# Kernel tuning notes

Hardware: AMD Instinct MI355X
Metric: run time of the kernel (lower is better)

The kernel has to match this reference:

```python
import jax, jax.numpy as jnp
import numpy as np

NUM_HEADS = 8
CH_PER_HEAD = 32
NUM_GROUPS = 32
EPS = 1e-5
SCALE = CH_PER_HEAD ** (-0.25)


def group_norm(x, scale, bias):
    # x: [b, c, h, w]
    b, c, h, w = x.shape
    xg = x.reshape(b, NUM_GROUPS, c // NUM_GROUPS, h, w)
    mean = xg.mean(axis=(2, 3, 4), keepdims=True)
    var = xg.var(axis=(2, 3, 4), keepdims=True)
    xg = (xg - mean) * jax.lax.rsqrt(var + EPS)
    x = xg.reshape(b, c, h, w)
    return x * scale[None, :, None, None] + bias[None, :, None, None]


def conv1x1(x, w, b):
    # x: [b, c_in, n], w: [c_out, c_in], b: [c_out]
    return jnp.einsum('oc,bcn->bon', w, x) + b[None, :, None]


def setup_inputs() -> dict:
    key = jax.random.key(0)
    ks = jax.random.split(key, 12)
    c_in, c_out, hid = 256, 256, NUM_HEADS * CH_PER_HEAD
    d = {}
    d['x'] = jax.random.normal(ks[0], (2, c_in, 64, 64), dtype=jnp.float32)
    d['gn_scale'] = jnp.ones((c_in,), dtype=jnp.float32)
    d['gn_bias'] = jnp.zeros((c_in,), dtype=jnp.float32)
    def lin(k, co, ci):
        return jax.random.normal(k, (co, ci), dtype=jnp.float32) * (ci ** -0.5)
    d['wq'] = lin(ks[1], hid, c_in)
    d['bq'] = jnp.zeros((hid,), dtype=jnp.float32)
    d['wk'] = lin(ks[2], hid, c_in)
    d['bk'] = jnp.zeros((hid,), dtype=jnp.float32)
    d['wv'] = lin(ks[3], hid, c_in)
    d['bv'] = jnp.zeros((hid,), dtype=jnp.float32)
    # Original zero-inits to_out; we use small random weights so the
    # attention path contributes to the output (non-trivial baseline).
    d['wo'] = lin(ks[4], c_out, hid) * 0.02
    d['bo'] = jnp.zeros((c_out,), dtype=jnp.float32)
    return d


def reference(x, gn_scale, gn_bias, wq, bq, wk, bk, wv, bv, wo, bo):
    b, c, h, w = x.shape
    n = h * w
    x_n = group_norm(x, gn_scale, gn_bias).reshape(b, c, n)
    q = conv1x1(x_n, wq, bq)  # [b, hid, n]
    k = conv1x1(x_n, wk, bk)
    v = conv1x1(x_n, wv, bv)
    def split_heads(t):
        return t.reshape(b, NUM_HEADS, CH_PER_HEAD, n)
    q, k, v = split_heads(q) * SCALE, split_heads(k) * SCALE, split_heads(v)
    attn = jax.nn.softmax(jnp.einsum('bhdi,bhdj->bhij', q, k), axis=-1)
    out = jnp.einsum('bhij,bhdj->bhdi', attn, v)  # [b, h, d, n]
    out = out.reshape(b, NUM_HEADS * CH_PER_HEAD, n)
    out = conv1x1(out, wo, bo).reshape(b, -1, h, w)
    return x + out
```

## Files before the change

### kernel.cpp

```cpp
#include <hip/hip_runtime.h>

#define C 256
#define N 4096
#define CPG 8
#define GE (CPG * N)
#define JL 2048

constexpr float EPS = 1e-5f;
constexpr float QK_SCALE_E = 0.50500979f;

typedef float f32x4 __attribute__((ext_vector_type(4)));
typedef short s16x8 __attribute__((ext_vector_type(8)));

__device__ __forceinline__ short f2bf(float f) {
    union { float f; unsigned u; } v; v.f = f;
    unsigned r = v.u + 0x7FFFu + ((v.u >> 16) & 1u);
    return (short)(r >> 16);
}
__device__ __forceinline__ float bf2f(short s) {
    union { unsigned u; float f; } v; v.u = ((unsigned)(unsigned short)s) << 16;
    return v.f;
}

__global__ __launch_bounds__(1024) void k_stats(const float* __restrict__ x,
                                                float2* __restrict__ stats) {
    int b = blockIdx.x >> 5, g = blockIdx.x & 31;
    size_t base = (size_t)(b * C + g * CPG) * N;
    const float* xp = x + base;
    int tid = threadIdx.x;
    float sum = 0.f, ss = 0.f;
    for (int i = tid * 4; i < GE; i += 4096) {
        float4 v = *(const float4*)(xp + i);
        sum += (v.x + v.y) + (v.z + v.w);
        ss  += (v.x * v.x + v.y * v.y) + (v.z * v.z + v.w * v.w);
    }
    #pragma unroll
    for (int o = 32; o; o >>= 1) {
        sum += __shfl_down(sum, o, 64);
        ss  += __shfl_down(ss, o, 64);
    }
    __shared__ float red[32];
    int wid = tid >> 6;
    if ((tid & 63) == 0) { red[wid] = sum; red[16 + wid] = ss; }
    __syncthreads();
    if (tid == 0) {
        sum = 0.f; ss = 0.f;
        #pragma unroll
        for (int i = 0; i < 16; ++i) { sum += red[i]; ss += red[16 + i]; }
        float mean = sum * (1.f / GE);
        float var  = ss * (1.f / GE) - mean * mean;
        stats[b * 32 + g] = make_float2(mean, rsqrtf(var + EPS));
    }
}

__global__ __launch_bounds__(256) void k_wcvt(const float* __restrict__ wq,
        const float* __restrict__ wk, const float* __restrict__ wv,
        const float* __restrict__ wo, short* __restrict__ wqkvb,
        short* __restrict__ wob) {
    int i = blockIdx.x * 256 + threadIdx.x;
    if (i < 65536)       wqkvb[i] = f2bf(wq[i]);
    else if (i < 131072) wqkvb[i] = f2bf(wk[i - 65536]);
    else if (i < 196608) wqkvb[i] = f2bf(wv[i - 131072]);
    else                 wob[i - 196608] = f2bf(wo[i - 196608]);
}

__global__ __launch_bounds__(256) void k_t(const float* __restrict__ x,
        const float* __restrict__ gs, const float* __restrict__ gb,
        const float2* __restrict__ stats, short* __restrict__ xnT) {
    __shared__ __align__(16) short lt[64][72];
    int id = blockIdx.x;
    int b  = id >> 8;
    int ct = (id >> 6) & 3;
    int nt = id & 63;
    int c0 = ct * 64, n0 = nt * 64;
    int t = threadIdx.x;
    int cc = t >> 2;
    int c = c0 + cc;
    float2 st = stats[b * 32 + (c >> 3)];
    float sc = gs[c] * st.y;
    float bi = gb[c] - st.x * sc;
    const float* xp = x + (size_t)(b * C + c) * N + n0;
    #pragma unroll
    for (int it = 0; it < 4; ++it) {
        int f4 = (t & 3) + it * 4;
        float4 v = *(const float4*)(xp + f4 * 4);
        int nl = f4 * 4;
        lt[nl + 0][cc] = f2bf(v.x * sc + bi);
        lt[nl + 1][cc] = f2bf(v.y * sc + bi);
        lt[nl + 2][cc] = f2bf(v.z * sc + bi);
        lt[nl + 3][cc] = f2bf(v.w * sc + bi);
    }
    __syncthreads();
    int nl = t >> 2, seg = t & 3;
    short* op = xnT + (size_t)(b * N + n0 + nl) * C + c0 + seg * 16;
    s16x8 w0 = *(const s16x8*)&lt[nl][seg * 16];
    s16x8 w1 = *(const s16x8*)&lt[nl][seg * 16 + 8];
    *(s16x8*)op = w0;
    *(s16x8*)(op + 8) = w1;
}

__global__ __launch_bounds__(256) void k_qkv(const short* __restrict__ wqkvb,
        const short* __restrict__ xnT, const float* __restrict__ bq,
        const float* __restrict__ bk, const float* __restrict__ bv,
        short* __restrict__ qT, short* __restrict__ kT, short* __restrict__ vB) {
    __shared__ __align__(16) short lt[4][64][16];
    int nb = blockIdx.x, mb = blockIdx.y, b = blockIdx.z;
    int m0 = mb * 64, n0 = nb * 64;
    int wid = threadIdx.x >> 6, lane = threadIdx.x & 63;
    int lr = lane & 15, lg = lane >> 4;
    int mw = m0 + wid * 16;
    const short* ap_ = wqkvb + (mw + lr) * C + lg * 8;
    const short* bp_ = xnT + ((size_t)b * N + n0 + lr) * C + lg * 8;
    f32x4 acc[4] = {{0,0,0,0},{0,0,0,0},{0,0,0,0},{0,0,0,0}};
    #pragma unroll 4
    for (int k0 = 0; k0 < C; k0 += 32) {
        s16x8 a  = *(const s16x8*)(ap_ + k0);
        s16x8 x0 = *(const s16x8*)(bp_ + k0);
        s16x8 x1 = *(const s16x8*)(bp_ + 16 * C + k0);
        s16x8 x2 = *(const s16x8*)(bp_ + 32 * C + k0);
        s16x8 x3 = *(const s16x8*)(bp_ + 48 * C + k0);
        acc[0] = __builtin_amdgcn_mfma_f32_16x16x32_bf16(a, x0, acc[0], 0, 0, 0);
        acc[1] = __builtin_amdgcn_mfma_f32_16x16x32_bf16(a, x1, acc[1], 0, 0, 0);
        acc[2] = __builtin_amdgcn_mfma_f32_16x16x32_bf16(a, x2, acc[2], 0, 0, 0);
        acc[3] = __builtin_amdgcn_mfma_f32_16x16x32_bf16(a, x3, acc[3], 0, 0, 0);
    }
    int kind = mb >> 2;
    const float* bias = kind == 0 ? bq : (kind == 1 ? bk : bv);
    int mloc = mw - kind * 256;
    float bvals[4];
    #pragma unroll
    for (int r = 0; r < 4; ++r) bvals[r] = bias[mloc + 4 * lg + r];
    int h = mloc >> 5;
    if (kind == 2) {
        short* vbase = vB + (size_t)((b * 8 + h) * 32) * N;
        #pragma unroll
        for (int f = 0; f < 4; ++f) {
            int n = n0 + f * 16 + lr;
            #pragma unroll
            for (int r = 0; r < 4; ++r) {
                int dd = (mloc & 31) + 4 * lg + r;
                vbase[(size_t)dd * N + n] = f2bf(acc[f][r] + bvals[r]);
            }
        }
    } else {
        short* dst = (kind == 0) ? qT : kT;
        #pragma unroll
        for (int f = 0; f < 4; ++f)
            #pragma unroll
            for (int r = 0; r < 4; ++r)
                lt[wid][f * 16 + lr][4 * lg + r] =
                    f2bf((acc[f][r] + bvals[r]) * QK_SCALE_E);
        int ln = lane;
        s16x8 w0 = *(const s16x8*)&lt[wid][ln][0];
        s16x8 w1 = *(const s16x8*)&lt[wid][ln][8];
        short* op = dst + ((size_t)(b * 8 + h) * N + n0 + ln) * 32 + (mloc & 16);
        *(s16x8*)op = w0;
        *(s16x8*)(op + 8) = w1;
    }
}

#define EXPB(d, s_) asm("v_exp_f32 %0, %1\n\ts_nop 0" : "=v"(d) : "v"(s_))

#define TILE_BODY() do {                                                          \
    f32x4 s0 = __builtin_amdgcn_mfma_f32_16x16x32_bf16(bk0, aq, zero, 0, 0, 0);   \
    f32x4 s1 = __builtin_amdgcn_mfma_f32_16x16x32_bf16(bk1, aq, zero, 0, 0, 0);   \
    float e00, e01, e02, e03, e10, e11, e12, e13;                                 \
    EXPB(e00, s0[0]); EXPB(e01, s0[1]); EXPB(e02, s0[2]); EXPB(e03, s0[3]);       \
    EXPB(e10, s1[0]); EXPB(e11, s1[1]); EXPB(e12, s1[2]); EXPB(e13, s1[3]);       \
    unsigned w0, w1, w2, w3;                                                      \
    asm("v_cvt_pk_bf16_f32 %0, %1, %2" : "=v"(w0) : "v"(e00), "v"(e01));          \
    asm("v_cvt_pk_bf16_f32 %0, %1, %2" : "=v"(w1) : "v"(e02), "v"(e03));          \
    asm("v_cvt_pk_bf16_f32 %0, %1, %2" : "=v"(w2) : "v"(e10), "v"(e11));          \
    asm("v_cvt_pk_bf16_f32 %0, %1, %2" : "=v"(w3) : "v"(e12), "v"(e13));          \
    asm("v_permlane32_swap_b32 %0, %1" : "+v"(w0), "+v"(w2));                     \
    asm("v_permlane16_swap_b32 %0, %1" : "+v"(w0), "+v"(w2));                     \
    asm("v_permlane32_swap_b32 %0, %1" : "+v"(w1), "+v"(w3));                     \
    asm("v_permlane16_swap_b32 %0, %1" : "+v"(w1), "+v"(w3));                     \
    union { int4 i4; s16x8 s8; } apu;                                             \
    apu.i4 = make_int4((int)w0, (int)w1, (int)w2, (int)w3);                       \
    s16x8 ap = apu.s8;                                                            \
    lac = __builtin_amdgcn_mfma_f32_16x16x32_bf16(ap, ones, lac, 0, 0, 0);        \
    o0  = __builtin_amdgcn_mfma_f32_16x16x32_bf16(ap, bv0, o0, 0, 0, 0);          \
    o1  = __builtin_amdgcn_mfma_f32_16x16x32_bf16(ap, bv1, o1, 0, 0, 0);          \
} while (0)

__global__ __launch_bounds__(256, 8) void k_attn(const short* __restrict__ qT,
        const short* __restrict__ kT, const short* __restrict__ vB,
        short* __restrict__ po0, short* __restrict__ po1,
        float* __restrict__ pl) {
    __shared__ __align__(16) short pool[8192];
    int xb  = blockIdx.x;
    int rm  = (xb & 7) * 128 + (xb >> 3);
    int bh  = rm >> 6;
    int wid = threadIdx.x >> 6;
    int i0  = (rm & 63) * 64 + wid * 16;
    int s   = blockIdx.y;
    int jb  = s * JL;
    int lane = threadIdx.x & 63;
    int lr = lane & 15, lg = lane >> 4;
    const short* qTb = qT + (size_t)bh * N * 32;
    const short* kTb = kT + (size_t)bh * N * 32;
    const short* vBb = vB + (size_t)bh * 32 * N;

    s16x8 aq = *(const s16x8*)(qTb + (i0 + lr) * 32 + lg * 8);
    s16x8 ones;
    #pragma unroll
    for (int e = 0; e < 8; ++e) ones[e] = (short)0x3F80;

    f32x4 o0 = {0,0,0,0}, o1 = {0,0,0,0}, lac = {0,0,0,0};
    const f32x4 zero = {0,0,0,0};

    int krow  = 16 * wid + (lane >> 2);
    int kslot = lane & 3;
    const short* kg = kTb + (size_t)(jb + krow) * 32 + kslot * 8;
    int kw_ofs = krow * 32 + ((kslot ^ (krow & 3)) * 8);

    int vrow  = 8 * wid + (lane >> 3);
    int vslot = lane & 7;
    const short* vg = vBb + (size_t)vrow * N + jb + vslot * 8;
    int vw_ofs = vrow * 64 + ((vslot ^ (vrow & 7)) * 8);

    int kr_base = lr * 32 + ((lg ^ (lr & 3)) * 8);
    int vr0 = lr * 64, vr1 = (16 + lr) * 64;
    int sw0 = ((0 + lg) ^ (lr & 7)) * 8;
    int sw1 = ((4 + lg) ^ (lr & 7)) * 8;

    {
        s16x8 kreg = *(const s16x8*)kg;
        s16x8 vreg = *(const s16x8*)vg;
        *(s16x8*)&pool[kw_ofs] = kreg;
        *(s16x8*)&pool[4096 + vw_ofs] = vreg;
    }
    __syncthreads();

    for (int t = 0; t < 32; ++t) {
        int p = t & 1;
        s16x8 nk, nv;
        if (t < 31) {
            nk = *(const s16x8*)(kg + (t + 1) * 2048);
            nv = *(const s16x8*)(vg + (t + 1) * 64);
        }
        const short* lkp = &pool[p * 2048];
        const short* lvp = &pool[4096 + p * 2048];
        {
            s16x8 bk0 = *(const s16x8*)(lkp + kr_base);
            s16x8 bk1 = *(const s16x8*)(lkp + 512 + kr_base);
            s16x8 bv0 = *(const s16x8*)(lvp + vr0 + sw0);
            s16x8 bv1 = *(const s16x8*)(lvp + vr1 + sw0);
            TILE_BODY();
        }
        {
            s16x8 bk0 = *(const s16x8*)(lkp + 1024 + kr_base);
            s16x8 bk1 = *(const s16x8*)(lkp + 1536 + kr_base);
            s16x8 bv0 = *(const s16x8*)(lvp + vr0 + sw1);
            s16x8 bv1 = *(const s16x8*)(lvp + vr1 + sw1);
            TILE_BODY();
        }
        if (t < 31) {
            int q = (t + 1) & 1;
            *(s16x8*)&pool[q * 2048 + kw_ofs] = nk;
            *(s16x8*)&pool[4096 + q * 2048 + vw_ofs] = nv;
        }
        __syncthreads();
    }

    #pragma unroll
    for (int r = 0; r < 4; ++r) {
        pool[wid * 640 + (4 * lg + r) * 40 + lr]      = f2bf(o0[r]);
        pool[wid * 640 + (4 * lg + r) * 40 + 16 + lr] = f2bf(o1[r]);
    }
    if (lr == 0) {
        float* plp = pl + ((size_t)(s * 16 + bh)) * N + i0;
        #pragma unroll
        for (int r = 0; r < 4; ++r) plp[4 * lg + r] = lac[r];
    }
    short* pob = s ? po1 : po0;
    int il = lane >> 2, seg = lane & 3;
    s16x8 w = *(const s16x8*)&pool[wid * 640 + il * 40 + seg * 8];
    short* op = pob + ((size_t)bh * N + i0 + il) * 32 + seg * 8;
    *(s16x8*)op = w;
}

__global__ __launch_bounds__(256) void k_merge(short* __restrict__ po0,
        const short* __restrict__ po1, const float* __restrict__ pl) {
    int idx = blockIdx.x * 256 + threadIdx.x;
    int dseg = idx & 3, i = (idx >> 2) & 4095, bh = idx >> 14;
    float l = pl[(size_t)bh * N + i] + pl[(size_t)(16 + bh) * N + i];
    float inv = 1.f / l;
    size_t off = ((size_t)bh * N + i) * 32 + dseg * 8;
    s16x8 a  = *(const s16x8*)(po0 + off);
    s16x8 c2 = *(const s16x8*)(po1 + off);
    s16x8 w;
    #pragma unroll
    for (int e = 0; e < 8; ++e)
        w[e] = f2bf((bf2f(a[e]) + bf2f(c2[e])) * inv);
    *(s16x8*)(po0 + off) = w;
}

__global__ __launch_bounds__(256) void k_out(const short* __restrict__ wob,
        const short* __restrict__ aoM, const float* __restrict__ bo,
        const float* __restrict__ x, float* __restrict__ out) {
    int nb = blockIdx.x, mb = blockIdx.y, b = blockIdx.z;
    int n0 = nb * 64;
    int wid = threadIdx.x >> 6, lane = threadIdx.x & 63;
    int lr = lane & 15, lg = lane >> 4;
    int mw = mb * 64 + wid * 16;
    const short* ap_ = wob + (mw + lr) * C + lg * 8;
    f32x4 acc[4] = {{0,0,0,0},{0,0,0,0},{0,0,0,0},{0,0,0,0}};
    #pragma unroll
    for (int h = 0; h < 8; ++h) {
        const short* bp = aoM + (((size_t)(b * 8 + h)) * N + n0 + lr) * 32 + lg * 8;
        s16x8 a  = *(const s16x8*)(ap_ + h * 32);
        s16x8 x0 = *(const s16x8*)(bp);
        s16x8 x1 = *(const s16x8*)(bp + 16 * 32);
        s16x8 x2 = *(const s16x8*)(bp + 32 * 32);
        s16x8 x3 = *(const s16x8*)(bp + 48 * 32);
        acc[0] = __builtin_amdgcn_mfma_f32_16x16x32_bf16(a, x0, acc[0], 0, 0, 0);
        acc[1] = __builtin_amdgcn_mfma_f32_16x16x32_bf16(a, x1, acc[1], 0, 0, 0);
        acc[2] = __builtin_amdgcn_mfma_f32_16x16x32_bf16(a, x2, acc[2], 0, 0, 0);
        acc[3] = __builtin_amdgcn_mfma_f32_16x16x32_bf16(a, x3, acc[3], 0, 0, 0);
    }
    float bvals[4];
    #pragma unroll
    for (int r = 0; r < 4; ++r) bvals[r] = bo[mw + 4 * lg + r];
    #pragma unroll
    for (int f = 0; f < 4; ++f) {
        int n = n0 + f * 16 + lr;
        #pragma unroll
        for (int r = 0; r < 4; ++r) {
            size_t idx = (size_t)(b * C + mw + 4 * lg + r) * N + n;
            out[idx] = acc[f][r] + bvals[r] + x[idx];
        }
    }
}

extern "C" void kernel_launch(void* const* d_in, const int* in_sizes, int n_in,
                              void* d_out, int out_size, void* d_ws, size_t ws_size,
                              hipStream_t stream) {
    const float* x  = (const float*)d_in[0];
    const float* gs = (const float*)d_in[1];
    const float* gb = (const float*)d_in[2];
    const float* wq = (const float*)d_in[3];
    const float* bq = (const float*)d_in[4];
    const float* wk = (const float*)d_in[5];
    const float* bk = (const float*)d_in[6];
    const float* wv = (const float*)d_in[7];
    const float* bv = (const float*)d_in[8];
    const float* wo = (const float*)d_in[9];
    const float* bo = (const float*)d_in[10];
    float* out = (float*)d_out;
    char* ws = (char*)d_ws;

    float2* stats = (float2*)(ws);
    short*  wqkvb = (short*)(ws + 0x1000);
    float*  pl    = (float*)(ws + 0x1000);
    short*  wob   = (short*)(ws + 0x81000);
    short*  xnT   = (short*)(ws + 0xB0000);
    short*  po1   = (short*)(ws + 0xB0000);
    short*  qT    = (short*)(ws + 0x4B0000);
    short*  kT    = (short*)(ws + 0x8B0000);
    short*  vB    = (short*)(ws + 0xCB0000);
    short*  po0   = (short*)(ws + 0x10B0000);

    k_stats<<<64, 1024, 0, stream>>>(x, stats);
    k_wcvt <<<1024, 256, 0, stream>>>(wq, wk, wv, wo, wqkvb, wob);
    k_t    <<<512, 256, 0, stream>>>(x, gs, gb, stats, xnT);
    k_qkv  <<<dim3(64, 12, 2), 256, 0, stream>>>(wqkvb, xnT, bq, bk, bv, qT, kT, vB);
    k_attn <<<dim3(1024, 2), 256, 0, stream>>>(qT, kT, vB, po0, po1, pl);
    k_merge<<<1024, 256, 0, stream>>>(po0, po1, pl);
    k_out  <<<dim3(64, 4, 2), 256, 0, stream>>>(wob, po0, bo, x, out);
}
```

Before: 182.6 us.

## Fuse split-attention merge into output projection and stage GEMM B tiles in LDS

```diff
diff --git a/kernel.cpp b/kernel.cpp
--- a/kernel.cpp
+++ b/kernel.cpp
@@ -103,27 +103,45 @@
         const short* __restrict__ xnT, const float* __restrict__ bq,
         const float* __restrict__ bk, const float* __restrict__ bv,
         short* __restrict__ qT, short* __restrict__ kT, short* __restrict__ vB) {
+    __shared__ __align__(16) short bs[64 * 256];
     __shared__ __align__(16) short lt[4][64][16];
     int nb = blockIdx.x, mb = blockIdx.y, b = blockIdx.z;
     int m0 = mb * 64, n0 = nb * 64;
-    int wid = threadIdx.x >> 6, lane = threadIdx.x & 63;
+    int t = threadIdx.x;
+    int wid = t >> 6, lane = t & 63;
     int lr = lane & 15, lg = lane >> 4;
     int mw = m0 + wid * 16;
+
     const short* ap_ = wqkvb + (mw + lr) * C + lg * 8;
-    const short* bp_ = xnT + ((size_t)b * N + n0 + lr) * C + lg * 8;
+    s16x8 af[8];
+    #pragma unroll
+    for (int kk = 0; kk < 8; ++kk)
+        af[kk] = *(const s16x8*)(ap_ + kk * 32);
+
+    {
+        int gr = t >> 2;
+        const short* gp = xnT + ((size_t)b * N + n0 + gr) * C + (t & 3) * 8;
+        #pragma unroll
+        for (int i = 0; i < 8; ++i) {
+            int sl = (t & 3) + 4 * i;
+            s16x8 v = *(const s16x8*)(gp + 32 * i);
+            *(s16x8*)&bs[gr * 256 + ((sl ^ (gr & 7)) * 8)] = v;
+        }
+    }
+    __syncthreads();
+
     f32x4 acc[4] = {{0,0,0,0},{0,0,0,0},{0,0,0,0},{0,0,0,0}};
-    #pragma unroll 4
-    for (int k0 = 0; k0 < C; k0 += 32) {
-        s16x8 a  = *(const s16x8*)(ap_ + k0);
-        s16x8 x0 = *(const s16x8*)(bp_ + k0);
-        s16x8 x1 = *(const s16x8*)(bp_ + 16 * C + k0);
-        s16x8 x2 = *(const s16x8*)(bp_ + 32 * C + k0);
-        s16x8 x3 = *(const s16x8*)(bp_ + 48 * C + k0);
-        acc[0] = __builtin_amdgcn_mfma_f32_16x16x32_bf16(a, x0, acc[0], 0, 0, 0);
-        acc[1] = __builtin_amdgcn_mfma_f32_16x16x32_bf16(a, x1, acc[1], 0, 0, 0);
-        acc[2] = __builtin_amdgcn_mfma_f32_16x16x32_bf16(a, x2, acc[2], 0, 0, 0);
-        acc[3] = __builtin_amdgcn_mfma_f32_16x16x32_bf16(a, x3, acc[3], 0, 0, 0);
-    }
+    #pragma unroll
+    for (int kk = 0; kk < 8; ++kk) {
+        int sb = kk * 4;
+        #pragma unroll
+        for (int f = 0; f < 4; ++f) {
+            int row = f * 16 + lr;
+            s16x8 xf = *(const s16x8*)&bs[row * 256 + (((sb + lg) ^ (lr & 7)) * 8)];
+            acc[f] = __builtin_amdgcn_mfma_f32_16x16x32_bf16(af[kk], xf, acc[f], 0, 0, 0);
+        }
+    }
+
     int kind = mb >> 2;
     const float* bias = kind == 0 ? bq : (kind == 1 ? bk : bv);
     int mloc = mw - kind * 256;
@@ -281,45 +299,58 @@
     *(s16x8*)op = w;
 }
 
-__global__ __launch_bounds__(256) void k_merge(short* __restrict__ po0,
-        const short* __restrict__ po1, const float* __restrict__ pl) {
-    int idx = blockIdx.x * 256 + threadIdx.x;
-    int dseg = idx & 3, i = (idx >> 2) & 4095, bh = idx >> 14;
-    float l = pl[(size_t)bh * N + i] + pl[(size_t)(16 + bh) * N + i];
-    float inv = 1.f / l;
-    size_t off = ((size_t)bh * N + i) * 32 + dseg * 8;
-    s16x8 a  = *(const s16x8*)(po0 + off);
-    s16x8 c2 = *(const s16x8*)(po1 + off);
-    s16x8 w;
-    #pragma unroll
-    for (int e = 0; e < 8; ++e)
-        w[e] = f2bf((bf2f(a[e]) + bf2f(c2[e])) * inv);
-    *(s16x8*)(po0 + off) = w;
-}
-
 __global__ __launch_bounds__(256) void k_out(const short* __restrict__ wob,
-        const short* __restrict__ aoM, const float* __restrict__ bo,
+        const short* __restrict__ po0, const short* __restrict__ po1,
+        const float* __restrict__ pl, const float* __restrict__ bo,
         const float* __restrict__ x, float* __restrict__ out) {
+    __shared__ __align__(16) short bs[8 * 64 * 32];
     int nb = blockIdx.x, mb = blockIdx.y, b = blockIdx.z;
     int n0 = nb * 64;
-    int wid = threadIdx.x >> 6, lane = threadIdx.x & 63;
+    int t = threadIdx.x;
+    int wid = t >> 6, lane = t & 63;
     int lr = lane & 15, lg = lane >> 4;
     int mw = mb * 64 + wid * 16;
+
     const short* ap_ = wob + (mw + lr) * C + lg * 8;
+    s16x8 af[8];
+    #pragma unroll
+    for (int h = 0; h < 8; ++h) af[h] = *(const s16x8*)(ap_ + h * 32);
+
+    {
+        int h = t >> 5, idx = t & 31;
+        size_t rb = ((size_t)(b * 8 + h)) * N + n0;
+        const short* g0 = po0 + rb * 32;
+        const short* g1 = po1 + rb * 32;
+        const float* pl0 = pl + rb;
+        const float* pl1 = pl + (size_t)16 * N * 16 / 16 * 1;
+        pl1 = pl + ((size_t)(16 + b * 8 + h)) * N + n0;
+        #pragma unroll
+        for (int i = 0; i < 8; ++i) {
+            int chunk = idx + 32 * i;
+            int r = chunk >> 2, sl = chunk & 3;
+            s16x8 v0 = *(const s16x8*)(g0 + r * 32 + sl * 8);
+            s16x8 v1 = *(const s16x8*)(g1 + r * 32 + sl * 8);
+            float inv = 1.f / (pl0[r] + pl1[r]);
+            s16x8 w;
+            #pragma unroll
+            for (int e = 0; e < 8; ++e)
+                w[e] = f2bf((bf2f(v0[e]) + bf2f(v1[e])) * inv);
+            *(s16x8*)&bs[h * 2048 + r * 32 + ((sl ^ (r & 3)) * 8)] = w;
+        }
+    }
+    __syncthreads();
+
     f32x4 acc[4] = {{0,0,0,0},{0,0,0,0},{0,0,0,0},{0,0,0,0}};
     #pragma unroll
     for (int h = 0; h < 8; ++h) {
-        const short* bp = aoM + (((size_t)(b * 8 + h)) * N + n0 + lr) * 32 + lg * 8;
-        s16x8 a  = *(const s16x8*)(ap_ + h * 32);
-        s16x8 x0 = *(const s16x8*)(bp);
-        s16x8 x1 = *(const s16x8*)(bp + 16 * 32);
-        s16x8 x2 = *(const s16x8*)(bp + 32 * 32);
-        s16x8 x3 = *(const s16x8*)(bp + 48 * 32);
-        acc[0] = __builtin_amdgcn_mfma_f32_16x16x32_bf16(a, x0, acc[0], 0, 0, 0);
-        acc[1] = __builtin_amdgcn_mfma_f32_16x16x32_bf16(a, x1, acc[1], 0, 0, 0);
-        acc[2] = __builtin_amdgcn_mfma_f32_16x16x32_bf16(a, x2, acc[2], 0, 0, 0);
-        acc[3] = __builtin_amdgcn_mfma_f32_16x16x32_bf16(a, x3, acc[3], 0, 0, 0);
-    }
+        #pragma unroll
+        for (int f = 0; f < 4; ++f) {
+            int row = f * 16 + lr;
+            s16x8 xf = *(const s16x8*)&bs[h * 2048 + row * 32 + ((lg ^ (lr & 3)) * 8)];
+            acc[f] = __builtin_amdgcn_mfma_f32_16x16x32_bf16(af[h], xf, acc[f], 0, 0, 0);
+        }
+    }
+
     float bvals[4];
     #pragma unroll
     for (int r = 0; r < 4; ++r) bvals[r] = bo[mw + 4 * lg + r];
@@ -367,6 +398,5 @@
     k_t    <<<512, 256, 0, stream>>>(x, gs, gb, stats, xnT);
     k_qkv  <<<dim3(64, 12, 2), 256, 0, stream>>>(wqkvb, xnT, bq, bk, bv, qT, kT, vB);
     k_attn <<<dim3(1024, 2), 256, 0, stream>>>(qT, kT, vB, po0, po1, pl);
-    k_merge<<<1024, 256, 0, stream>>>(po0, po1, pl);
-    k_out  <<<dim3(64, 4, 2), 256, 0, stream>>>(wob, po0, bo, x, out);
-}
+    k_out  <<<dim3(64, 4, 2), 256, 0, stream>>>(wob, po0, po1, pl, bo, x, out);
+}
```

Result: faster. 165.2 us (-9.5%).
